# Performance work log

Measured on AMD Instinct MI355X. Metric: run time of the kernel, lower is better.

The kernel has to match this reference:

```python
import jax, jax.numpy as jnp
import numpy as np

B, C, H, W = 4, 256, 64, 64
E = C // 8  # embedding_channels = inChannels // k


def setup_inputs() -> dict:
    key = jax.random.key(0)
    ks = jax.random.split(key, 9)
    sc = 1.0 / np.sqrt(C)
    so = 1.0 / np.sqrt(E)
    return {
        "x": jax.random.normal(ks[0], (B, C, H, W), dtype=jnp.float32),
        "Wk": jax.random.normal(ks[1], (E, C), dtype=jnp.float32) * sc,
        "bk": jax.random.normal(ks[2], (E,), dtype=jnp.float32) * 0.01,
        "Wq": jax.random.normal(ks[3], (E, C), dtype=jnp.float32) * sc,
        "bq": jax.random.normal(ks[4], (E,), dtype=jnp.float32) * 0.01,
        "Wv": jax.random.normal(ks[5], (E, C), dtype=jnp.float32) * sc,
        "bv": jax.random.normal(ks[6], (E,), dtype=jnp.float32) * 0.01,
        "Wo": jax.random.normal(ks[7], (C, E), dtype=jnp.float32) * so,
        "bo": jax.random.normal(ks[8], (C,), dtype=jnp.float32) * 0.01,
    }


def reference(x, Wk, bk, Wq, bq, Wv, bv, Wo, bo):
    b, c, h, w = x.shape
    n = h * w
    gamma = jnp.float32(0.5)  # non-learned branch (learned=False default)

    def conv1x1(inp, Wt, bt):
        # 1x1 conv == channel-mixing matmul: [b,c,h,w] x [e,c] -> [b,e,h,w]
        return jnp.einsum('bchw,ec->behw', inp, Wt) + bt[None, :, None, None]

    f = conv1x1(x, Wk, bk).reshape(b, -1, n)  # key   [b,E,N]
    g = conv1x1(x, Wq, bq).reshape(b, -1, n)  # query [b,E,N]
    hx = conv1x1(x, Wv, bv).reshape(b, -1, n)  # value [b,E,N]

    s = jnp.einsum('bei,bej->bij', f, g)       # f^T @ g, [b,N,N]
    beta = jax.nn.softmax(s, axis=1)           # softmax over dim 1 (rows) as in torch
    v = jnp.einsum('bei,bij->bej', hx, beta)   # h @ beta, [b,E,N]
    v = v.reshape(b, -1, h, w)

    o = jnp.einsum('behw,ce->bchw', v, Wo) + bo[None, :, None, None]
    y = gamma * o + x
    return y, o, gamma
```

## Files before the change

kernel.cpp:

```cpp
#include <hip/hip_runtime.h>

#define B_ 4
#define C_ 256
#define N_ 4096
#define E_ 32

typedef _Float16 f16x8 __attribute__((ext_vector_type(8)));
typedef _Float16 f16x4 __attribute__((ext_vector_type(4)));
typedef float f32x4 __attribute__((ext_vector_type(4)));

#define LOG2E 1.44269504088896f

__global__ __launch_bounds__(256) void proj_kernel(
    const float* __restrict__ x,
    const float* __restrict__ Wk, const float* __restrict__ bk,
    const float* __restrict__ Wq, const float* __restrict__ bq,
    const float* __restrict__ Wv, const float* __restrict__ bv,
    const float* __restrict__ Wo,
    _Float16* __restrict__ Qb, _Float16* __restrict__ Kb, _Float16* __restrict__ Vb,
    _Float16* __restrict__ Wof16, float* __restrict__ out)
{
    const int m = blockIdx.x >> 8;
    if (m == 3) {
        for (int i4 = threadIdx.x; i4 < (C_ * E_) / 4; i4 += 256) {
            float4 wv = ((const float4*)Wo)[i4];
            f16x4 tp = {(_Float16)wv.x, (_Float16)wv.y, (_Float16)wv.z, (_Float16)wv.w};
            *(f16x4*)&Wof16[i4 * 4] = tp;
        }
        if (threadIdx.x == 0)
            out[(size_t)2 * B_ * C_ * N_] = 0.5f;
        return;
    }
    const int rem = blockIdx.x & 255;
    const int b   = rem >> 6;
    const int n0  = (rem & 63) << 6;
    const int t    = threadIdx.x;
    const int lane = t & 63;
    const int wave = t >> 6;
    const int l15  = lane & 15;
    const int quad = lane >> 4;

    __shared__ _Float16 xT[64][264];
    __shared__ _Float16 Wl[32][264];

    const float* W    = (m == 0) ? Wk : (m == 1) ? Wq : Wv;
    const float* bias = (m == 0) ? bk : (m == 1) ? bq : bv;

    for (int i4 = t; i4 < (E_ * C_) / 4; i4 += 256) {
        float4 wv = ((const float4*)W)[i4];
        int e = (i4 * 4) >> 8, c = (i4 * 4) & 255;
        f16x4 tp = {(_Float16)wv.x, (_Float16)wv.y, (_Float16)wv.z, (_Float16)wv.w};
        *(f16x4*)&Wl[e][c] = tp;
    }
    for (int i4 = t; i4 < (64 * 256) / 4; i4 += 256) {
        int j4 = (i4 & 15) * 4;
        int c  = i4 >> 4;
        float4 xv = *(const float4*)(x + (size_t)(b * C_ + c) * N_ + n0 + j4);
        xT[j4 + 0][c] = (_Float16)xv.x;
        xT[j4 + 1][c] = (_Float16)xv.y;
        xT[j4 + 2][c] = (_Float16)xv.z;
        xT[j4 + 3][c] = (_Float16)xv.w;
    }
    __syncthreads();

    f16x8 Bf[8];
    for (int kk = 0; kk < 8; ++kk)
        Bf[kk] = *(const f16x8*)&xT[wave * 16 + l15][kk * 32 + quad * 8];

    const float sc = (m == 1) ? LOG2E : 1.0f;
    for (int et = 0; et < 2; ++et) {
        f32x4 acc = {0.f, 0.f, 0.f, 0.f};
        for (int kk = 0; kk < 8; ++kk) {
            f16x8 Af = *(const f16x8*)&Wl[et * 16 + l15][kk * 32 + quad * 8];
            acc = __builtin_amdgcn_mfma_f32_16x16x32_f16(Af, Bf[kk], acc, 0, 0, 0);
        }
        const int n = n0 + wave * 16 + l15;
        for (int r = 0; r < 4; ++r) {
            const int e = et * 16 + quad * 4 + r;
            float v = (acc[r] + bias[e]) * sc;
            _Float16 hv = (_Float16)v;
            if      (m == 0) Kb[(size_t)(b * N_ + n) * E_ + e] = hv;
            else if (m == 1) Qb[(size_t)(b * N_ + n) * E_ + e] = hv;
            else             Vb[(size_t)(b * E_ + e) * N_ + n] = hv;
        }
    }
}

__global__ __launch_bounds__(512, 6) void attn_kernel(
    const _Float16* __restrict__ Qb, const _Float16* __restrict__ Kb,
    const _Float16* __restrict__ Vb, const _Float16* __restrict__ Wof16,
    const float* __restrict__ bo, const float* __restrict__ x,
    float* __restrict__ out)
{
    const int wave = threadIdx.x >> 6;
    const int lane = threadIdx.x & 63;
    const int l15  = lane & 15, quad = lane >> 4;
    const int jg   = blockIdx.x;
    const int b    = jg >> 8;
    const int j0   = (jg & 255) << 4;

    __shared__ __align__(16) char pbuf[8][2176];
    __shared__ float    mls[8][2][16];
    __shared__ _Float16 Om[16][40];

    _Float16 (*pb)[40] = (_Float16 (*)[40])(pbuf[wave]);

    f16x8 Qf = *(const f16x8*)(Qb + (size_t)(b * N_ + j0 + l15) * E_ + quad * 8);

    f32x4 O0 = {0, 0, 0, 0}, O1 = {0, 0, 0, 0};
    float mrow = -1e30f, lsum = 0.f;

    const _Float16* Kp  = Kb + (size_t)b * N_ * E_ + (size_t)(wave << 9) * E_;
    const _Float16* Vp  = Vb + (size_t)b * E_ * N_ + (wave << 9);

    for (int it = 0; it < 16; ++it) {
        const int i0 = it * 32;
        f16x8 K0 = *(const f16x8*)(Kp + (size_t)(i0 + l15) * E_ + quad * 8);
        f16x8 K1 = *(const f16x8*)(Kp + (size_t)(i0 + 16 + l15) * E_ + quad * 8);
        f16x8 Va = *(const f16x8*)(Vp + (size_t)l15 * N_ + i0 + quad * 8);
        f16x8 Vc = *(const f16x8*)(Vp + (size_t)(16 + l15) * N_ + i0 + quad * 8);
        f32x4 z = {0, 0, 0, 0};
        f32x4 S0 = __builtin_amdgcn_mfma_f32_16x16x32_f16(K0, Qf, z, 0, 0, 0);
        f32x4 S1 = __builtin_amdgcn_mfma_f32_16x16x32_f16(K1, Qf, z, 0, 0, 0);
        float a0 = fmaxf(S0[0], S0[1]), a1 = fmaxf(S0[2], S0[3]);
        float a2 = fmaxf(S1[0], S1[1]), a3 = fmaxf(S1[2], S1[3]);
        float mx = fmaxf(fmaxf(a0, a1), fmaxf(a2, a3));
        mx = fmaxf(mx, __shfl_xor(mx, 16));
        mx = fmaxf(mx, __shfl_xor(mx, 32));
        float mnew  = fmaxf(mrow, mx);
        float alpha = exp2f(mrow - mnew);
        mrow = mnew;
        float p00 = exp2f(S0[0] - mnew), p01 = exp2f(S0[1] - mnew);
        float p02 = exp2f(S0[2] - mnew), p03 = exp2f(S0[3] - mnew);
        float p10 = exp2f(S1[0] - mnew), p11 = exp2f(S1[1] - mnew);
        float p12 = exp2f(S1[2] - mnew), p13 = exp2f(S1[3] - mnew);
        float ps = ((p00 + p01) + (p02 + p03)) + ((p10 + p11) + (p12 + p13));
        lsum = lsum * alpha + ps;
        for (int r = 0; r < 4; ++r) { O0[r] *= alpha; O1[r] *= alpha; }
        f16x4 w0 = {(_Float16)p00, (_Float16)p01, (_Float16)p02, (_Float16)p03};
        f16x4 w1 = {(_Float16)p10, (_Float16)p11, (_Float16)p12, (_Float16)p13};
        *(f16x4*)&pb[l15][quad * 4]      = w0;
        *(f16x4*)&pb[l15][16 + quad * 4] = w1;
        f16x8 P = *(const f16x8*)&pb[l15][quad * 8];
        O0 = __builtin_amdgcn_mfma_f32_16x16x32_f16(Va, P, O0, 0, 0, 0);
        O1 = __builtin_amdgcn_mfma_f32_16x16x32_f16(Vc, P, O1, 0, 0, 0);
    }

    lsum += __shfl_xor(lsum, 16);
    lsum += __shfl_xor(lsum, 32);
    if (quad == 0) { mls[wave][0][l15] = mrow; mls[wave][1][l15] = lsum; }
    __syncthreads();

    float M = -1e30f, ms[8], ls[8];
    for (int s = 0; s < 8; ++s) {
        ms[s] = mls[s][0][l15]; ls[s] = mls[s][1][l15];
        M = fmaxf(M, ms[s]);
    }
    float L = 0.f;
    for (int s = 0; s < 8; ++s) L += ls[s] * exp2f(ms[s] - M);
    const float w = exp2f(mrow - M) / L;

    float (*osum)[34] = (float (*)[34])(pbuf[wave]);
    *(f32x4*)&osum[l15][quad * 4]      = O0 * w;
    *(f32x4*)&osum[l15][16 + quad * 4] = O1 * w;
    __syncthreads();

    {
        const int j = threadIdx.x >> 5;
        const int e = threadIdx.x & 31;
        float a = 0.f;
        for (int s = 0; s < 8; ++s)
            a += ((const float (*)[34])(pbuf[s]))[j][e];
        Om[j][e] = (_Float16)a;
    }
    __syncthreads();

    f16x8 Bf2 = *(const f16x8*)&Om[l15][quad * 8];
    float* out_y = out + (size_t)b * C_ * N_;
    float* out_o = out + (size_t)B_ * C_ * N_ + (size_t)b * C_ * N_;
    const float* xb = x + (size_t)b * C_ * N_;
    for (int ct = 0; ct < 2; ++ct) {
        const int c0 = wave * 32 + ct * 16;
        f16x8 Af = *(const f16x8*)(Wof16 + (size_t)(c0 + l15) * E_ + quad * 8);
        f32x4 z = {0, 0, 0, 0};
        f32x4 acc = __builtin_amdgcn_mfma_f32_16x16x32_f16(Af, Bf2, z, 0, 0, 0);
        for (int r = 0; r < 4; ++r) {
            const int c = c0 + quad * 4 + r;
            size_t idx = (size_t)c * N_ + j0 + l15;
            float ov = acc[r] + bo[c];
            out_o[idx] = ov;
            out_y[idx] = 0.5f * ov + xb[idx];
        }
    }
}

extern "C" void kernel_launch(void* const* d_in, const int* in_sizes, int n_in,
                              void* d_out, int out_size, void* d_ws, size_t ws_size,
                              hipStream_t stream)
{
    const float* x  = (const float*)d_in[0];
    const float* Wk = (const float*)d_in[1];
    const float* bk = (const float*)d_in[2];
    const float* Wq = (const float*)d_in[3];
    const float* bq = (const float*)d_in[4];
    const float* Wv = (const float*)d_in[5];
    const float* bv = (const float*)d_in[6];
    const float* Wo = (const float*)d_in[7];
    const float* bo = (const float*)d_in[8];
    float* out = (float*)d_out;

    char* ws = (char*)d_ws;
    _Float16* Qb    = (_Float16*)(ws);
    _Float16* Kb    = (_Float16*)(ws + (1u << 20));
    _Float16* Vb    = (_Float16*)(ws + (2u << 20));
    _Float16* Wof16 = (_Float16*)(ws + (3u << 20));

    proj_kernel<<<dim3(3 * B_ * (N_ / 64) + 256), dim3(256), 0, stream>>>(
        x, Wk, bk, Wq, bq, Wv, bv, Wo, Qb, Kb, Vb, Wof16, out);
    attn_kernel<<<dim3(B_ * (N_ / 16)), dim3(512), 0, stream>>>(
        Qb, Kb, Vb, Wof16, bo, x, out);
}
```

Before: 148.5 us.

## Prefetch K/V, drop LDS P relayout, lazy softmax rescale, swizzle proj LDS

The attention loop now loads the next K/V tiles while computing the current one. It feeds the softmax probabilities directly from registers into 16x16x16 MFMAs instead of round-tripping through shared memory. The running max is updated only when it grows by more than 8 (log2 units), which skips most rescale multiplies. In the projection kernel the transposed x tile is XOR-swizzled to cut bank conflicts, K/Q stores are vectorized, and the grid launches a single block for Wo conversion instead of 256. The lazy rescale lets unnormalized probabilities grow up to 256 in fp16, which adds some precision risk.

```diff
diff --git a/kernel.cpp b/kernel.cpp
--- a/kernel.cpp
+++ b/kernel.cpp
@@ -10,6 +10,8 @@
 typedef float f32x4 __attribute__((ext_vector_type(4)));
 
 #define LOG2E 1.44269504088896f
+
+#define XSWZ(row, col) ((col) ^ ((((row) >> 2) & 7) << 3))
 
 __global__ __launch_bounds__(256) void proj_kernel(
     const float* __restrict__ x,
@@ -56,16 +58,17 @@
         int j4 = (i4 & 15) * 4;
         int c  = i4 >> 4;
         float4 xv = *(const float4*)(x + (size_t)(b * C_ + c) * N_ + n0 + j4);
-        xT[j4 + 0][c] = (_Float16)xv.x;
-        xT[j4 + 1][c] = (_Float16)xv.y;
-        xT[j4 + 2][c] = (_Float16)xv.z;
-        xT[j4 + 3][c] = (_Float16)xv.w;
-    }
-    __syncthreads();
-
+        xT[j4 + 0][XSWZ(j4 + 0, c)] = (_Float16)xv.x;
+        xT[j4 + 1][XSWZ(j4 + 1, c)] = (_Float16)xv.y;
+        xT[j4 + 2][XSWZ(j4 + 2, c)] = (_Float16)xv.z;
+        xT[j4 + 3][XSWZ(j4 + 3, c)] = (_Float16)xv.w;
+    }
+    __syncthreads();
+
+    const int row = wave * 16 + l15;
     f16x8 Bf[8];
     for (int kk = 0; kk < 8; ++kk)
-        Bf[kk] = *(const f16x8*)&xT[wave * 16 + l15][kk * 32 + quad * 8];
+        Bf[kk] = *(const f16x8*)&xT[row][XSWZ(row, kk * 32 + quad * 8)];
 
     const float sc = (m == 1) ? LOG2E : 1.0f;
     for (int et = 0; et < 2; ++et) {
@@ -74,14 +77,18 @@
             f16x8 Af = *(const f16x8*)&Wl[et * 16 + l15][kk * 32 + quad * 8];
             acc = __builtin_amdgcn_mfma_f32_16x16x32_f16(Af, Bf[kk], acc, 0, 0, 0);
         }
-        const int n = n0 + wave * 16 + l15;
-        for (int r = 0; r < 4; ++r) {
-            const int e = et * 16 + quad * 4 + r;
-            float v = (acc[r] + bias[e]) * sc;
-            _Float16 hv = (_Float16)v;
-            if      (m == 0) Kb[(size_t)(b * N_ + n) * E_ + e] = hv;
-            else if (m == 1) Qb[(size_t)(b * N_ + n) * E_ + e] = hv;
-            else             Vb[(size_t)(b * E_ + e) * N_ + n] = hv;
+        const int n  = n0 + wave * 16 + l15;
+        const int e0 = et * 16 + quad * 4;
+        if (m == 2) {
+            for (int r = 0; r < 4; ++r)
+                Vb[(size_t)(b * E_ + e0 + r) * N_ + n] =
+                    (_Float16)(acc[r] + bias[e0 + r]);
+        } else {
+            f16x4 st;
+            for (int r = 0; r < 4; ++r)
+                st[r] = (_Float16)((acc[r] + bias[e0 + r]) * sc);
+            _Float16* dst = (m == 0) ? Kb : Qb;
+            *(f16x4*)&dst[(size_t)(b * N_ + n) * E_ + e0] = st;
         }
     }
 }
@@ -103,47 +110,59 @@
     __shared__ float    mls[8][2][16];
     __shared__ _Float16 Om[16][40];
 
-    _Float16 (*pb)[40] = (_Float16 (*)[40])(pbuf[wave]);
-
     f16x8 Qf = *(const f16x8*)(Qb + (size_t)(b * N_ + j0 + l15) * E_ + quad * 8);
 
     f32x4 O0 = {0, 0, 0, 0}, O1 = {0, 0, 0, 0};
     float mrow = -1e30f, lsum = 0.f;
 
-    const _Float16* Kp  = Kb + (size_t)b * N_ * E_ + (size_t)(wave << 9) * E_;
-    const _Float16* Vp  = Vb + (size_t)b * E_ * N_ + (wave << 9);
+    const _Float16* Kp = Kb + (size_t)b * N_ * E_ + (size_t)(wave << 9) * E_;
+    const _Float16* Vp = Vb + (size_t)b * E_ * N_ + (wave << 9);
+
+    f16x8 K0  = *(const f16x8*)(Kp + (size_t)l15 * E_ + quad * 8);
+    f16x8 K1  = *(const f16x8*)(Kp + (size_t)(16 + l15) * E_ + quad * 8);
+    f16x4 Va0 = *(const f16x4*)(Vp + (size_t)l15 * N_ + quad * 4);
+    f16x4 Va1 = *(const f16x4*)(Vp + (size_t)l15 * N_ + 16 + quad * 4);
+    f16x4 Vc0 = *(const f16x4*)(Vp + (size_t)(16 + l15) * N_ + quad * 4);
+    f16x4 Vc1 = *(const f16x4*)(Vp + (size_t)(16 + l15) * N_ + 16 + quad * 4);
 
     for (int it = 0; it < 16; ++it) {
-        const int i0 = it * 32;
-        f16x8 K0 = *(const f16x8*)(Kp + (size_t)(i0 + l15) * E_ + quad * 8);
-        f16x8 K1 = *(const f16x8*)(Kp + (size_t)(i0 + 16 + l15) * E_ + quad * 8);
-        f16x8 Va = *(const f16x8*)(Vp + (size_t)l15 * N_ + i0 + quad * 8);
-        f16x8 Vc = *(const f16x8*)(Vp + (size_t)(16 + l15) * N_ + i0 + quad * 8);
         f32x4 z = {0, 0, 0, 0};
         f32x4 S0 = __builtin_amdgcn_mfma_f32_16x16x32_f16(K0, Qf, z, 0, 0, 0);
         f32x4 S1 = __builtin_amdgcn_mfma_f32_16x16x32_f16(K1, Qf, z, 0, 0, 0);
-        float a0 = fmaxf(S0[0], S0[1]), a1 = fmaxf(S0[2], S0[3]);
-        float a2 = fmaxf(S1[0], S1[1]), a3 = fmaxf(S1[2], S1[3]);
-        float mx = fmaxf(fmaxf(a0, a1), fmaxf(a2, a3));
+        const int i0n = ((it + 1) & 15) << 5;
+        K0 = *(const f16x8*)(Kp + (size_t)(i0n + l15) * E_ + quad * 8);
+        K1 = *(const f16x8*)(Kp + (size_t)(i0n + 16 + l15) * E_ + quad * 8);
+
+        float mx = fmaxf(fmaxf(fmaxf(S0[0], S0[1]), fmaxf(S0[2], S0[3])),
+                         fmaxf(fmaxf(S1[0], S1[1]), fmaxf(S1[2], S1[3])));
         mx = fmaxf(mx, __shfl_xor(mx, 16));
         mx = fmaxf(mx, __shfl_xor(mx, 32));
-        float mnew  = fmaxf(mrow, mx);
-        float alpha = exp2f(mrow - mnew);
-        mrow = mnew;
-        float p00 = exp2f(S0[0] - mnew), p01 = exp2f(S0[1] - mnew);
-        float p02 = exp2f(S0[2] - mnew), p03 = exp2f(S0[3] - mnew);
-        float p10 = exp2f(S1[0] - mnew), p11 = exp2f(S1[1] - mnew);
-        float p12 = exp2f(S1[2] - mnew), p13 = exp2f(S1[3] - mnew);
-        float ps = ((p00 + p01) + (p02 + p03)) + ((p10 + p11) + (p12 + p13));
-        lsum = lsum * alpha + ps;
-        for (int r = 0; r < 4; ++r) { O0[r] *= alpha; O1[r] *= alpha; }
-        f16x4 w0 = {(_Float16)p00, (_Float16)p01, (_Float16)p02, (_Float16)p03};
-        f16x4 w1 = {(_Float16)p10, (_Float16)p11, (_Float16)p12, (_Float16)p13};
-        *(f16x4*)&pb[l15][quad * 4]      = w0;
-        *(f16x4*)&pb[l15][16 + quad * 4] = w1;
-        f16x8 P = *(const f16x8*)&pb[l15][quad * 8];
-        O0 = __builtin_amdgcn_mfma_f32_16x16x32_f16(Va, P, O0, 0, 0, 0);
-        O1 = __builtin_amdgcn_mfma_f32_16x16x32_f16(Vc, P, O1, 0, 0, 0);
+        if (__any(mx > mrow + 8.f)) {
+            float mnew  = fmaxf(mrow, mx);
+            float alpha = exp2f(mrow - mnew);
+            mrow = mnew;
+            lsum *= alpha;
+            O0 *= alpha;
+            O1 *= alpha;
+        }
+        float p00 = exp2f(S0[0] - mrow), p01 = exp2f(S0[1] - mrow);
+        float p02 = exp2f(S0[2] - mrow), p03 = exp2f(S0[3] - mrow);
+        float p10 = exp2f(S1[0] - mrow), p11 = exp2f(S1[1] - mrow);
+        float p12 = exp2f(S1[2] - mrow), p13 = exp2f(S1[3] - mrow);
+        lsum += ((p00 + p01) + (p02 + p03)) + ((p10 + p11) + (p12 + p13));
+
+        f16x4 P0 = {(_Float16)p00, (_Float16)p01, (_Float16)p02, (_Float16)p03};
+        f16x4 P1 = {(_Float16)p10, (_Float16)p11, (_Float16)p12, (_Float16)p13};
+
+        O0 = __builtin_amdgcn_mfma_f32_16x16x16f16(Va0, P0, O0, 0, 0, 0);
+        O1 = __builtin_amdgcn_mfma_f32_16x16x16f16(Vc0, P0, O1, 0, 0, 0);
+        O0 = __builtin_amdgcn_mfma_f32_16x16x16f16(Va1, P1, O0, 0, 0, 0);
+        O1 = __builtin_amdgcn_mfma_f32_16x16x16f16(Vc1, P1, O1, 0, 0, 0);
+
+        Va0 = *(const f16x4*)(Vp + (size_t)l15 * N_ + i0n + quad * 4);
+        Va1 = *(const f16x4*)(Vp + (size_t)l15 * N_ + i0n + 16 + quad * 4);
+        Vc0 = *(const f16x4*)(Vp + (size_t)(16 + l15) * N_ + i0n + quad * 4);
+        Vc1 = *(const f16x4*)(Vp + (size_t)(16 + l15) * N_ + i0n + 16 + quad * 4);
     }
 
     lsum += __shfl_xor(lsum, 16);
@@ -215,7 +234,7 @@
     _Float16* Vb    = (_Float16*)(ws + (2u << 20));
     _Float16* Wof16 = (_Float16*)(ws + (3u << 20));
 
-    proj_kernel<<<dim3(3 * B_ * (N_ / 64) + 256), dim3(256), 0, stream>>>(
+    proj_kernel<<<dim3(3 * B_ * (N_ / 64) + 1), dim3(256), 0, stream>>>(
         x, Wk, bk, Wq, bq, Wv, bv, Wo, Qb, Kb, Vb, Wof16, out);
     attn_kernel<<<dim3(B_ * (N_ / 16)), dim3(512), 0, stream>>>(
         Qb, Kb, Vb, Wof16, bo, x, out);
```

After: 171.9 us. +15.8%, slower.
